# Performance work log

Measured on AMD Instinct MI355X. Metric: run time of the kernel, lower is better.

## Reference

```python
import jax, jax.numpy as jnp
import numpy as np

N_NODES = 50000
N_EDGES = 800000
D = 128  # hidden_dim == node feature dim


def setup_inputs() -> dict:
    key = jax.random.key(0)
    k1, k2, k3, k4 = jax.random.split(key, 4)
    node_feat = jax.random.normal(k1, (N_NODES, D), dtype=jnp.float32)
    edge_index = jax.random.randint(k2, (2, N_EDGES), 0, N_NODES, dtype=jnp.int32)
    # MLP params: LazyLinear(2D -> D), Linear(D -> D)
    W1 = jax.random.normal(k3, (2 * D, D), dtype=jnp.float32) * (1.0 / np.sqrt(2 * D))
    b1 = jnp.zeros((D,), dtype=jnp.float32)
    W2 = jax.random.normal(k4, (D, D), dtype=jnp.float32) * (1.0 / np.sqrt(D))
    b2 = jnp.zeros((D,), dtype=jnp.float32)
    return {"node_feat": node_feat, "edge_index": edge_index,
            "W1": W1, "b1": b1, "W2": W2, "b2": b2}


def reference(node_feat, edge_index, W1, b1, W2, b2):
    # node_feat: [N, D]; edge_index: [2, E]
    src, dst = edge_index[0], edge_index[1]
    n = node_feat.shape[0]
    # gather source feats [E, D], scatter-add into dst -> [N, D]
    msgs = node_feat[src]
    agg = jax.ops.segment_sum(msgs, dst, num_segments=n)
    # degree normalization (clamp min 1)
    deg = jax.ops.segment_sum(jnp.ones_like(dst, dtype=node_feat.dtype), dst,
                              num_segments=n)
    agg = agg / jnp.maximum(deg, 1.0)[:, None]
    # update MLP on concat([node_feat, agg]); dropout is identity at eval
    h = jnp.concatenate([node_feat, agg], axis=-1)          # [N, 2D]
    h = jax.nn.relu(h @ W1 + b1)                             # [N, D]
    h = jax.nn.relu(h @ W2 + b2)                             # [N, D]
    return h
```

## Files before the change

kernel.cpp:

```cpp
#include <hip/hip_runtime.h>
#include <hip/hip_bf16.h>

#define N_NODES 50000
#define N_EDGES 800000
#define D 128
#define SLOTS 64
#define NTILES 782

typedef __attribute__((ext_vector_type(8))) short short8v;
typedef __attribute__((ext_vector_type(4))) float f32x4;


__device__ __forceinline__ unsigned short f32_to_bf16_rn(float f) {
    unsigned int u = __float_as_uint(f);
    unsigned int r = (u + 0x7fffu + ((u >> 16) & 1u)) >> 16;
    return (unsigned short)r;
}
__device__ __forceinline__ unsigned int pack2(float a, float b) {
    return (unsigned int)f32_to_bf16_rn(a) |
           ((unsigned int)f32_to_bf16_rn(b) << 16);
}
__device__ __forceinline__ float bflo(unsigned int w) {
    return __uint_as_float(w << 16);
}
__device__ __forceinline__ float bfhi(unsigned int w) {
    return __uint_as_float(w & 0xffff0000u);
}

__global__ __launch_bounds__(256) void build_kernel(
    const int* __restrict__ ei, const float* __restrict__ x,
    const float* __restrict__ W1, const float* __restrict__ W2,
    int* __restrict__ cnt, int* __restrict__ ss,
    unsigned short* __restrict__ xb, unsigned short* __restrict__ Wt1,
    unsigned short* __restrict__ Wt2) {
    const int XBW = N_NODES * D / 8;
    int tid = blockIdx.x * 256 + threadIdx.x;
    if (tid < N_EDGES) {
        int dst = ei[N_EDGES + tid];
        int pos = atomicAdd(&cnt[dst], 1);
        if (pos < SLOTS) ss[(size_t)dst * SLOTS + pos] = ei[tid];
    }
    int t1 = tid - N_EDGES;
    if (t1 >= 0 && t1 < XBW) {
        const float4* p = reinterpret_cast<const float4*>(x + (size_t)t1 * 8);
        float4 v0 = p[0], v1 = p[1];
        uint4 o;
        o.x = pack2(v0.x, v0.y);
        o.y = pack2(v0.z, v0.w);
        o.z = pack2(v1.x, v1.y);
        o.w = pack2(v1.z, v1.w);
        *reinterpret_cast<uint4*>(xb + (size_t)t1 * 8) = o;
    }
    int t2 = t1 - XBW;
    if (t2 >= 0 && t2 < 128 * 256) {
        int n = t2 >> 8, k = t2 & 255;
        Wt1[t2] = f32_to_bf16_rn(W1[k * 128 + n]);
    }
    int t3 = t2 - 128 * 256;
    if (t3 >= 0 && t3 < 128 * 128) {
        int n = t3 >> 7, k = t3 & 127;
        Wt2[t3] = f32_to_bf16_rn(W2[k * 128 + n]);
    }
}

__global__ __launch_bounds__(256) void aggregate_kernel(
    const unsigned short* __restrict__ xb, const int* __restrict__ cnt,
    const int* __restrict__ ss, unsigned short* __restrict__ ab) {
    const int lane = threadIdx.x & 63;
    const int row = blockIdx.x * 4 + (threadIdx.x >> 6);
    const int dg = cnt[row];
    const int* sp = ss + (size_t)row * SLOTS;
    float fx = 0.0f, fy = 0.0f;
    int j = 0;
    for (; j + 4 <= dg; j += 4) {
        int s0 = sp[j + 0];
        int s1 = sp[j + 1];
        int s2 = sp[j + 2];
        int s3 = sp[j + 3];
        unsigned int g0 = reinterpret_cast<const unsigned int*>(xb + (size_t)s0 * D)[lane];
        unsigned int g1 = reinterpret_cast<const unsigned int*>(xb + (size_t)s1 * D)[lane];
        unsigned int g2 = reinterpret_cast<const unsigned int*>(xb + (size_t)s2 * D)[lane];
        unsigned int g3 = reinterpret_cast<const unsigned int*>(xb + (size_t)s3 * D)[lane];
        fx += bflo(g0) + bflo(g1) + bflo(g2) + bflo(g3);
        fy += bfhi(g0) + bfhi(g1) + bfhi(g2) + bfhi(g3);
    }
    for (; j < dg; ++j) {
        int s0 = sp[j];
        unsigned int g0 = reinterpret_cast<const unsigned int*>(xb + (size_t)s0 * D)[lane];
        fx += bflo(g0);
        fy += bfhi(g0);
    }
    const float inv = 1.0f / fmaxf((float)dg, 1.0f);
    reinterpret_cast<unsigned int*>(ab + (size_t)row * D)[lane] =
        pack2(fx * inv, fy * inv);
}

__global__ __launch_bounds__(256, 1) void mlp_kernel(
    const unsigned short* __restrict__ xb, const unsigned short* __restrict__ ab,
    const unsigned short* __restrict__ Wt1,
    const unsigned short* __restrict__ Wt2, const float* __restrict__ b1,
    const float* __restrict__ b2, float* __restrict__ out) {
    __shared__ unsigned char w1s[65536];
    __shared__ unsigned char w2s[32768];
    __shared__ unsigned char h1t[4][4096];

    const int tid = threadIdx.x;
    for (int i = tid; i < 4096; i += 256) {
        unsigned o = (unsigned)i * 16;
        uint4 v = reinterpret_cast<const uint4*>(Wt1)[i];
        *reinterpret_cast<uint4*>(w1s + (o ^ (((o >> 9) & 7u) << 4))) = v;
    }
    for (int i = tid; i < 2048; i += 256) {
        unsigned o = (unsigned)i * 16;
        uint4 v = reinterpret_cast<const uint4*>(Wt2)[i];
        *reinterpret_cast<uint4*>(w2s + (o ^ (((o >> 8) & 7u) << 4))) = v;
    }

    const int lane = tid & 63;
    const int wv = tid >> 6;
    const int rloc = lane & 15;
    const int kseg = lane >> 4;
    const unsigned rswz = (unsigned)((rloc & 7) << 4);
    unsigned char* my = h1t[wv];

    float bias1[8], bias2[8];
#pragma unroll
    for (int ct = 0; ct < 8; ++ct) {
        bias1[ct] = b1[ct * 16 + rloc];
        bias2[ct] = b2[ct * 16 + rloc];
    }
    __syncthreads();

    for (int tile = blockIdx.x; tile < NTILES; tile += gridDim.x) {
        const int rbase = tile * 64 + wv * 16;
        int arow = rbase + rloc;
        if (arow >= N_NODES) arow = N_NODES - 1;

        short8v a[8];
#pragma unroll
        for (int kk = 0; kk < 8; ++kk) {
            const unsigned short* ap =
                (kk < 4) ? xb + (size_t)arow * D + kk * 32 + kseg * 8
                         : ab + (size_t)arow * D + (kk - 4) * 32 + kseg * 8;
            a[kk] = *reinterpret_cast<const short8v*>(ap);
        }
        f32x4 acc[8];
#pragma unroll
        for (int ct = 0; ct < 8; ++ct) acc[ct] = (f32x4){0.f, 0.f, 0.f, 0.f};
#pragma unroll
        for (int kk = 0; kk < 8; ++kk) {
#pragma unroll
            for (int ct = 0; ct < 8; ++ct) {
                unsigned off = (unsigned)((ct * 16 + rloc) * 512 + kk * 64 + kseg * 16);
                short8v b = *reinterpret_cast<const short8v*>(w1s + (off ^ rswz));
                acc[ct] = __builtin_amdgcn_mfma_f32_16x16x32_bf16(a[kk], b, acc[ct], 0, 0, 0);
            }
        }
#pragma unroll
        for (int ct = 0; ct < 8; ++ct) {
#pragma unroll
            for (int r = 0; r < 4; ++r) {
                int lrow = kseg * 4 + r;
                float v = fmaxf(acc[ct][r] + bias1[ct], 0.0f);
                unsigned off = (unsigned)(lrow * 256 + (ct * 16 + rloc) * 2);
                *reinterpret_cast<unsigned short*>(
                    my + (off ^ ((unsigned)((lrow & 7) << 4)))) = f32_to_bf16_rn(v);
            }
        }
        __syncthreads();

        short8v a2[4];
#pragma unroll
        for (int kk = 0; kk < 4; ++kk) {
            unsigned off = (unsigned)(rloc * 256 + kk * 64 + kseg * 16);
            a2[kk] = *reinterpret_cast<const short8v*>(my + (off ^ rswz));
        }
        f32x4 acc2[8];
#pragma unroll
        for (int ct = 0; ct < 8; ++ct) acc2[ct] = (f32x4){0.f, 0.f, 0.f, 0.f};
#pragma unroll
        for (int kk = 0; kk < 4; ++kk) {
#pragma unroll
            for (int ct = 0; ct < 8; ++ct) {
                unsigned off = (unsigned)((ct * 16 + rloc) * 256 + kk * 64 + kseg * 16);
                short8v b = *reinterpret_cast<const short8v*>(w2s + (off ^ rswz));
                acc2[ct] = __builtin_amdgcn_mfma_f32_16x16x32_bf16(a2[kk], b, acc2[ct], 0, 0, 0);
            }
        }
        const int orow0 = rbase + kseg * 4;
#pragma unroll
        for (int ct = 0; ct < 8; ++ct) {
#pragma unroll
            for (int r = 0; r < 4; ++r) {
                int row = orow0 + r;
                if (row < N_NODES) {
                    out[(size_t)row * 128 + ct * 16 + rloc] =
                        fmaxf(acc2[ct][r] + bias2[ct], 0.0f);
                }
            }
        }
        __syncthreads();
    }
}

extern "C" void kernel_launch(void* const* d_in, const int* in_sizes, int n_in,
                              void* d_out, int out_size, void* d_ws,
                              size_t ws_size, hipStream_t stream) {
    const float* node_feat = (const float*)d_in[0];
    const int* ei = (const int*)d_in[1];
    const float* W1 = (const float*)d_in[2];
    const float* b1 = (const float*)d_in[3];
    const float* W2 = (const float*)d_in[4];
    const float* b2 = (const float*)d_in[5];
    float* out = (float*)d_out;

    int* cnt = (int*)d_ws;
    int* ss = cnt + N_NODES;
    unsigned short* xb = (unsigned short*)(ss + (size_t)N_NODES * SLOTS);
    unsigned short* ab = xb + (size_t)N_NODES * D;
    unsigned short* Wt1 = ab + (size_t)N_NODES * D;
    unsigned short* Wt2 = Wt1 + 128 * 256;

    const int XBW = N_NODES * D / 8;
    const int build_threads = N_EDGES + XBW + 128 * 256 + 128 * 128;

    hipMemsetAsync(cnt, 0, N_NODES * sizeof(int), stream);
    build_kernel<<<(build_threads + 255) / 256, 256, 0, stream>>>(
        ei, node_feat, W1, W2, cnt, ss, xb, Wt1, Wt2);
    aggregate_kernel<<<N_NODES / 4, 256, 0, stream>>>(xb, cnt, ss, ab);
    mlp_kernel<<<256, 256, 0, stream>>>(xb, ab, Wt1, Wt2, b1, b2, out);
}
```

Baseline: 126.4 us.

## Slice node features into column chunks for cache-local gather aggregation

Bf16 node features and aggregates are stored as 8 column slices of 16 values each, and aggregation runs one slice per block, so each gather pass touches a 1.6MB working set that fits in cache. Neighbor indices are stored as 16-bit values and shared across 8 lanes by shuffle, with one node per 8-lane group. The MLP kernel reads its A operands from the sliced layout. Storing indices as unsigned short truncates node ids up to 50000; that still fits in 16 bits, but it adds an extra kernel and more total gather instructions.

```diff
diff --git a/kernel.cpp b/kernel.cpp
--- a/kernel.cpp
+++ b/kernel.cpp
@@ -27,31 +27,19 @@
     return __uint_as_float(w & 0xffff0000u);
 }
 
-__global__ __launch_bounds__(256) void build_kernel(
-    const int* __restrict__ ei, const float* __restrict__ x,
-    const float* __restrict__ W1, const float* __restrict__ W2,
-    int* __restrict__ cnt, int* __restrict__ ss,
-    unsigned short* __restrict__ xb, unsigned short* __restrict__ Wt1,
+__global__ __launch_bounds__(256) void fill_kernel(
+    const int* __restrict__ ei, const float* __restrict__ W1,
+    const float* __restrict__ W2, int* __restrict__ cnt,
+    unsigned short* __restrict__ ss, unsigned short* __restrict__ Wt1,
     unsigned short* __restrict__ Wt2) {
-    const int XBW = N_NODES * D / 8;
     int tid = blockIdx.x * 256 + threadIdx.x;
     if (tid < N_EDGES) {
         int dst = ei[N_EDGES + tid];
         int pos = atomicAdd(&cnt[dst], 1);
-        if (pos < SLOTS) ss[(size_t)dst * SLOTS + pos] = ei[tid];
-    }
-    int t1 = tid - N_EDGES;
-    if (t1 >= 0 && t1 < XBW) {
-        const float4* p = reinterpret_cast<const float4*>(x + (size_t)t1 * 8);
-        float4 v0 = p[0], v1 = p[1];
-        uint4 o;
-        o.x = pack2(v0.x, v0.y);
-        o.y = pack2(v0.z, v0.w);
-        o.z = pack2(v1.x, v1.y);
-        o.w = pack2(v1.z, v1.w);
-        *reinterpret_cast<uint4*>(xb + (size_t)t1 * 8) = o;
-    }
-    int t2 = t1 - XBW;
+        if (pos < SLOTS)
+            ss[(size_t)dst * SLOTS + pos] = (unsigned short)ei[tid];
+    }
+    int t2 = tid - N_EDGES;
     if (t2 >= 0 && t2 < 128 * 256) {
         int n = t2 >> 8, k = t2 & 255;
         Wt1[t2] = f32_to_bf16_rn(W1[k * 128 + n]);
@@ -63,40 +51,69 @@
     }
 }
 
+__global__ __launch_bounds__(256) void prep_kernel(
+    const float* __restrict__ x, unsigned short* __restrict__ xcs) {
+    int n = blockIdx.x * 256 + threadIdx.x;
+    int cp = blockIdx.y;
+    if (n >= N_NODES) return;
+    const float4* p = reinterpret_cast<const float4*>(x + (size_t)n * D + cp * 32);
+    float4 v0 = p[0], v1 = p[1], v2 = p[2], v3 = p[3];
+    float4 w0 = p[4], w1 = p[5], w2 = p[6], w3 = p[7];
+    uint4 a0 = make_uint4(pack2(v0.x, v0.y), pack2(v0.z, v0.w),
+                          pack2(v1.x, v1.y), pack2(v1.z, v1.w));
+    uint4 a1 = make_uint4(pack2(v2.x, v2.y), pack2(v2.z, v2.w),
+                          pack2(v3.x, v3.y), pack2(v3.z, v3.w));
+    uint4 b0 = make_uint4(pack2(w0.x, w0.y), pack2(w0.z, w0.w),
+                          pack2(w1.x, w1.y), pack2(w1.z, w1.w));
+    uint4 b1 = make_uint4(pack2(w2.x, w2.y), pack2(w2.z, w2.w),
+                          pack2(w3.x, w3.y), pack2(w3.z, w3.w));
+    unsigned short* da = xcs + ((size_t)(2 * cp) * N_NODES + n) * 16;
+    unsigned short* db = xcs + ((size_t)(2 * cp + 1) * N_NODES + n) * 16;
+    reinterpret_cast<uint4*>(da)[0] = a0;
+    reinterpret_cast<uint4*>(da)[1] = a1;
+    reinterpret_cast<uint4*>(db)[0] = b0;
+    reinterpret_cast<uint4*>(db)[1] = b1;
+}
+
 __global__ __launch_bounds__(256) void aggregate_kernel(
-    const unsigned short* __restrict__ xb, const int* __restrict__ cnt,
-    const int* __restrict__ ss, unsigned short* __restrict__ ab) {
-    const int lane = threadIdx.x & 63;
-    const int row = blockIdx.x * 4 + (threadIdx.x >> 6);
-    const int dg = cnt[row];
-    const int* sp = ss + (size_t)row * SLOTS;
+    const unsigned short* __restrict__ xcs, const int* __restrict__ cnt,
+    const unsigned short* __restrict__ ss, unsigned short* __restrict__ acs) {
+    const int slice = blockIdx.x & 7;
+    const int chunk = blockIdx.x >> 3;
+    const int tid = threadIdx.x;
+    const int lane = tid & 63;
+    const int wv = tid >> 6;
+    const int grp = lane >> 3;
+    const int l8 = lane & 7;
+    const int gb = lane & ~7;
+    const int row = chunk * 32 + wv * 8 + grp;
+    if (row >= N_NODES) return;
+    int dg = __builtin_nontemporal_load(cnt + row);
+    if (dg > SLOTS) dg = SLOTS;
+    const unsigned short* sp = ss + (size_t)row * SLOTS;
+    const unsigned short* xs = xcs + (size_t)slice * N_NODES * 16;
     float fx = 0.0f, fy = 0.0f;
-    int j = 0;
-    for (; j + 4 <= dg; j += 4) {
-        int s0 = sp[j + 0];
-        int s1 = sp[j + 1];
-        int s2 = sp[j + 2];
-        int s3 = sp[j + 3];
-        unsigned int g0 = reinterpret_cast<const unsigned int*>(xb + (size_t)s0 * D)[lane];
-        unsigned int g1 = reinterpret_cast<const unsigned int*>(xb + (size_t)s1 * D)[lane];
-        unsigned int g2 = reinterpret_cast<const unsigned int*>(xb + (size_t)s2 * D)[lane];
-        unsigned int g3 = reinterpret_cast<const unsigned int*>(xb + (size_t)s3 * D)[lane];
-        fx += bflo(g0) + bflo(g1) + bflo(g2) + bflo(g3);
-        fy += bfhi(g0) + bfhi(g1) + bfhi(g2) + bfhi(g3);
-    }
-    for (; j < dg; ++j) {
-        int s0 = sp[j];
-        unsigned int g0 = reinterpret_cast<const unsigned int*>(xb + (size_t)s0 * D)[lane];
-        fx += bflo(g0);
-        fy += bfhi(g0);
+    for (int j = 0; j < dg; j += 8) {
+        int idv = 0;
+        if (j + l8 < dg) idv = (int)__builtin_nontemporal_load(sp + j + l8);
+        int m = dg - j;
+        if (m > 8) m = 8;
+        for (int k = 0; k < m; ++k) {
+            int s = __shfl(idv, gb + k);
+            unsigned int g =
+                reinterpret_cast<const unsigned int*>(xs + (size_t)s * 16)[l8];
+            fx += bflo(g);
+            fy += bfhi(g);
+        }
     }
     const float inv = 1.0f / fmaxf((float)dg, 1.0f);
-    reinterpret_cast<unsigned int*>(ab + (size_t)row * D)[lane] =
+    reinterpret_cast<unsigned int*>(acs +
+                                    ((size_t)slice * N_NODES + row) * 16)[l8] =
         pack2(fx * inv, fy * inv);
 }
 
 __global__ __launch_bounds__(256, 1) void mlp_kernel(
-    const unsigned short* __restrict__ xb, const unsigned short* __restrict__ ab,
+    const unsigned short* __restrict__ xcs, const unsigned short* __restrict__ acs,
     const unsigned short* __restrict__ Wt1,
     const unsigned short* __restrict__ Wt2, const float* __restrict__ b1,
     const float* __restrict__ b2, float* __restrict__ out) {
@@ -131,6 +148,7 @@
     }
     __syncthreads();
 
+    const int soff = (kseg & 1) * 8;
     for (int tile = blockIdx.x; tile < NTILES; tile += gridDim.x) {
         const int rbase = tile * 64 + wv * 16;
         int arow = rbase + rloc;
@@ -139,10 +157,10 @@
         short8v a[8];
 #pragma unroll
         for (int kk = 0; kk < 8; ++kk) {
-            const unsigned short* ap =
-                (kk < 4) ? xb + (size_t)arow * D + kk * 32 + kseg * 8
-                         : ab + (size_t)arow * D + (kk - 4) * 32 + kseg * 8;
-            a[kk] = *reinterpret_cast<const short8v*>(ap);
+            const unsigned short* base = (kk < 4) ? xcs : acs;
+            const int sl = ((kk & 3) * 2) + (kseg >> 1);
+            a[kk] = *reinterpret_cast<const short8v*>(
+                base + ((size_t)sl * N_NODES + arow) * 16 + soff);
         }
         f32x4 acc[8];
 #pragma unroll
@@ -215,18 +233,21 @@
     float* out = (float*)d_out;
 
     int* cnt = (int*)d_ws;
-    int* ss = cnt + N_NODES;
-    unsigned short* xb = (unsigned short*)(ss + (size_t)N_NODES * SLOTS);
-    unsigned short* ab = xb + (size_t)N_NODES * D;
-    unsigned short* Wt1 = ab + (size_t)N_NODES * D;
+    unsigned short* ss = (unsigned short*)(cnt + N_NODES);
+    unsigned short* xcs = ss + (size_t)N_NODES * SLOTS;
+    unsigned short* acs = xcs + (size_t)8 * N_NODES * 16;
+    unsigned short* Wt1 = acs + (size_t)8 * N_NODES * 16;
     unsigned short* Wt2 = Wt1 + 128 * 256;
 
-    const int XBW = N_NODES * D / 8;
-    const int build_threads = N_EDGES + XBW + 128 * 256 + 128 * 128;
+    const int fill_threads = N_EDGES + 128 * 256 + 128 * 128;
 
     hipMemsetAsync(cnt, 0, N_NODES * sizeof(int), stream);
-    build_kernel<<<(build_threads + 255) / 256, 256, 0, stream>>>(
-        ei, node_feat, W1, W2, cnt, ss, xb, Wt1, Wt2);
-    aggregate_kernel<<<N_NODES / 4, 256, 0, stream>>>(xb, cnt, ss, ab);
-    mlp_kernel<<<256, 256, 0, stream>>>(xb, ab, Wt1, Wt2, b1, b2, out);
-}
+    fill_kernel<<<(fill_threads + 255) / 256, 256, 0, stream>>>(
+        ei, W1, W2, cnt, ss, Wt1, Wt2);
+    {
+        dim3 g((N_NODES + 255) / 256, 4);
+        prep_kernel<<<g, 256, 0, stream>>>(node_feat, xcs);
+    }
+    aggregate_kernel<<<1563 * 8, 256, 0, stream>>>(xcs, cnt, ss, acs);
+    mlp_kernel<<<256, 256, 0, stream>>>(xcs, acs, Wt1, Wt2, b1, b2, out);
+}
```

New measurement: 168.3 us. +33.2%, slower.
